# Optimization experiments

Measured on AMD Instinct MI355X. Metric: run time of the kernel, lower is better.

The kernel has to match this reference:

```python
import jax, jax.numpy as jnp
import numpy as np

B, N, D = 8, 256, 256
LN_EPS = 1e-5


def setup_inputs() -> dict:
    key = jax.random.key(0)
    ks = jax.random.split(key, 8)
    s1 = 1.0 / np.sqrt(2 * D)  # torch Linear init scale ~ U(-1/sqrt(fan_in), ...); use normal*scale
    s2 = 1.0 / np.sqrt(D)
    return {
        "patch_features": jax.random.normal(ks[0], (B, N, D), dtype=jnp.float32),
        # relation_transform: Linear(2D, D) -> ReLU -> Linear(D, 1)
        "W1": jax.random.normal(ks[1], (2 * D, D), dtype=jnp.float32) * s1,
        "b1": jax.random.normal(ks[2], (D,), dtype=jnp.float32) * s1,
        "W2": jax.random.normal(ks[3], (D, 1), dtype=jnp.float32) * s2,
        "b2": jax.random.normal(ks[4], (1,), dtype=jnp.float32) * s2,
        # context_projection: Linear(D, D) + LayerNorm(D)
        "Wp": jax.random.normal(ks[5], (D, D), dtype=jnp.float32) * s2,
        "bp": jax.random.normal(ks[6], (D,), dtype=jnp.float32) * s2,
        "ln_gamma": jnp.ones((D,), dtype=jnp.float32),
        "ln_beta": jnp.zeros((D,), dtype=jnp.float32),
    }


def reference(patch_features, W1, b1, W2, b2, Wp, bp, ln_gamma, ln_beta):
    x = patch_features  # [B, N, D]
    d = x.shape[-1]
    # cat([x_i, x_j]) @ W1 == x_i @ W1[:D] + x_j @ W1[D:]
    hi = jnp.einsum("bnd,de->bne", x, W1[:d])   # [B, N, D]
    hj = jnp.einsum("bmd,de->bme", x, W1[d:])   # [B, N, D]
    h = jax.nn.relu(hi[:, :, None, :] + hj[:, None, :, :] + b1)  # [B, N, N, D]
    scores = jnp.einsum("bnmd,do->bnm", h, W2) + b2[0]            # [B, N, N]
    # diagonal entries stay exactly 0 (original never fills i == j)
    eye = jnp.eye(scores.shape[1], dtype=bool)
    scores = jnp.where(eye[None, :, :], 0.0, scores)
    weights = jax.nn.softmax(scores, axis=2)                      # [B, N, N]
    ctx = jnp.einsum("bnm,bmd->bnd", weights, x)                  # [B, N, D]
    proj = jnp.einsum("bnd,de->bne", ctx, Wp) + bp
    mu = jnp.mean(proj, axis=-1, keepdims=True)
    var = jnp.mean(jnp.square(proj - mu), axis=-1, keepdims=True)
    ln = (proj - mu) * jax.lax.rsqrt(var + LN_EPS) * ln_gamma + ln_beta
    return x + ln
```

## Files before the change

### kernel.cpp

```cpp
#include <hip/hip_runtime.h>

#define LN_EPS 1e-5f

__device__ __forceinline__ float wred_max(float v) {
#pragma unroll
    for (int off = 32; off; off >>= 1) v = fmaxf(v, __shfl_xor(v, off, 64));
    return v;
}
__device__ __forceinline__ float wred_sum(float v) {
#pragma unroll
    for (int off = 32; off; off >>= 1) v += __shfl_xor(v, off, 64);
    return v;
}


#define GL(Q, KB) { const float* _p = Wb + (size_t)((KB) * 8) * 256;            \
    _Pragma("unroll") for (int _j = 0; _j < 8; _j++)                            \
        Q[_j] = *(const float2*)(_p + (size_t)_j * 256); }

#define GC(Q, KB) { const int _k = (KB) * 8;                                    \
    _Pragma("unroll") for (int _r = 0; _r < 4; _r++) {                          \
        float4 _xa = *(const float4*)&xs[_r][_k];                               \
        float4 _xb = *(const float4*)&xs[_r][_k + 4];                           \
        acc[_r][0] = fmaf(_xa.x, Q[0].x, acc[_r][0]);                           \
        acc[_r][1] = fmaf(_xa.x, Q[0].y, acc[_r][1]);                           \
        acc[_r][0] = fmaf(_xa.y, Q[1].x, acc[_r][0]);                           \
        acc[_r][1] = fmaf(_xa.y, Q[1].y, acc[_r][1]);                           \
        acc[_r][0] = fmaf(_xa.z, Q[2].x, acc[_r][0]);                           \
        acc[_r][1] = fmaf(_xa.z, Q[2].y, acc[_r][1]);                           \
        acc[_r][0] = fmaf(_xa.w, Q[3].x, acc[_r][0]);                           \
        acc[_r][1] = fmaf(_xa.w, Q[3].y, acc[_r][1]);                           \
        acc[_r][0] = fmaf(_xb.x, Q[4].x, acc[_r][0]);                           \
        acc[_r][1] = fmaf(_xb.x, Q[4].y, acc[_r][1]);                           \
        acc[_r][0] = fmaf(_xb.y, Q[5].x, acc[_r][0]);                           \
        acc[_r][1] = fmaf(_xb.y, Q[5].y, acc[_r][1]);                           \
        acc[_r][0] = fmaf(_xb.z, Q[6].x, acc[_r][0]);                           \
        acc[_r][1] = fmaf(_xb.z, Q[6].y, acc[_r][1]);                           \
        acc[_r][0] = fmaf(_xb.w, Q[7].x, acc[_r][0]);                           \
        acc[_r][1] = fmaf(_xb.w, Q[7].y, acc[_r][1]); } }

__global__ __launch_bounds__(256) void k_gemm_hij(
    const float* __restrict__ x,
    const float* __restrict__ W1,
    const float* __restrict__ b1,
    float* __restrict__ hi_ws,
    float* __restrict__ hjT)
{
    __shared__ __align__(16) float xs[4][256];
    const int t = threadIdx.x;
    const int lane = t & 63, w = t >> 6;
    const int b = blockIdx.x & 7;
    const int i = blockIdx.x >> 3;
    const int row0 = b * 256 + i * 4;

    ((float4*)xs)[t] = ((const float4*)(x + (size_t)row0 * 256))[t];
    __syncthreads();

    const int half = w >> 1;
    const int e0 = ((w & 1) << 7) + 2 * lane;
    const float* Wb = W1 + (size_t)half * 65536 + e0;

    float acc[4][2];
#pragma unroll
    for (int r = 0; r < 4; r++) { acc[r][0] = 0.f; acc[r][1] = 0.f; }

    float2 q[3][8];
    GL(q[0], 0);
    GL(q[1], 1);
#pragma unroll
    for (int kb = 0; kb < 32; kb++) {
        if (kb + 2 < 32) GL(q[(kb + 2) % 3], kb + 2);
        GC(q[kb % 3], kb);
    }

    if (half == 0) {
        float2 bb = *(const float2*)(b1 + e0);
#pragma unroll
        for (int r = 0; r < 4; r++)
            *(float2*)&hi_ws[(size_t)(row0 + r) * 256 + e0] =
                make_float2(acc[r][0] + bb.x, acc[r][1] + bb.y);
    } else {
        const int m0 = i * 4;
        *(float4*)&hjT[(size_t)b * 65536 + (size_t)e0 * 256 + m0] =
            make_float4(acc[0][0], acc[1][0], acc[2][0], acc[3][0]);
        *(float4*)&hjT[(size_t)b * 65536 + (size_t)(e0 + 1) * 256 + m0] =
            make_float4(acc[0][1], acc[1][1], acc[2][1], acc[3][1]);
    }
}


#define P1L(H, G) { const float* _p = hjp + (size_t)((G) * 4) * 256;            \
    _Pragma("unroll") for (int _j = 0; _j < 4; _j++)                            \
        H[_j] = *(const float4*)(_p + (size_t)_j * 256); }

#define P1C(H, G) { const int _db = w * 64 + (G) * 4;                           \
    float4 _wq = *(const float4*)&w2_s[_db];                                    \
    _Pragma("unroll") for (int _n = 0; _n < 4; _n++) {                          \
        float4 _h4 = *(const float4*)&hi_s[_n][_db];                            \
        sp[_n][0] = fmaf(fmaxf(_h4.x + H[0].x, 0.f), _wq.x, sp[_n][0]);         \
        sp[_n][0] = fmaf(fmaxf(_h4.y + H[1].x, 0.f), _wq.y, sp[_n][0]);         \
        sp[_n][0] = fmaf(fmaxf(_h4.z + H[2].x, 0.f), _wq.z, sp[_n][0]);         \
        sp[_n][0] = fmaf(fmaxf(_h4.w + H[3].x, 0.f), _wq.w, sp[_n][0]);         \
        sp[_n][1] = fmaf(fmaxf(_h4.x + H[0].y, 0.f), _wq.x, sp[_n][1]);         \
        sp[_n][1] = fmaf(fmaxf(_h4.y + H[1].y, 0.f), _wq.y, sp[_n][1]);         \
        sp[_n][1] = fmaf(fmaxf(_h4.z + H[2].y, 0.f), _wq.z, sp[_n][1]);         \
        sp[_n][1] = fmaf(fmaxf(_h4.w + H[3].y, 0.f), _wq.w, sp[_n][1]);         \
        sp[_n][2] = fmaf(fmaxf(_h4.x + H[0].z, 0.f), _wq.x, sp[_n][2]);         \
        sp[_n][2] = fmaf(fmaxf(_h4.y + H[1].z, 0.f), _wq.y, sp[_n][2]);         \
        sp[_n][2] = fmaf(fmaxf(_h4.z + H[2].z, 0.f), _wq.z, sp[_n][2]);         \
        sp[_n][2] = fmaf(fmaxf(_h4.w + H[3].z, 0.f), _wq.w, sp[_n][2]);         \
        sp[_n][3] = fmaf(fmaxf(_h4.x + H[0].w, 0.f), _wq.x, sp[_n][3]);         \
        sp[_n][3] = fmaf(fmaxf(_h4.y + H[1].w, 0.f), _wq.y, sp[_n][3]);         \
        sp[_n][3] = fmaf(fmaxf(_h4.z + H[2].w, 0.f), _wq.z, sp[_n][3]);         \
        sp[_n][3] = fmaf(fmaxf(_h4.w + H[3].w, 0.f), _wq.w, sp[_n][3]); } }

#define DL4(X, PTR, G) { const float* _p = (PTR) + (size_t)((G) * 4) * 256;     \
    _Pragma("unroll") for (int _j = 0; _j < 4; _j++)                            \
        X[_j] = *(const float4*)(_p + (size_t)_j * 256); }

#define DC4(ACCV, WS, X, G) { const int _rb = w * 64 + (G) * 4;                 \
    _Pragma("unroll") for (int _n = 0; _n < 4; _n++) {                          \
        float4 _wa = *(const float4*)&WS[_n][_rb];                              \
        ACCV[_n][0] = fmaf(_wa.x, X[0].x, ACCV[_n][0]);                         \
        ACCV[_n][0] = fmaf(_wa.y, X[1].x, ACCV[_n][0]);                         \
        ACCV[_n][0] = fmaf(_wa.z, X[2].x, ACCV[_n][0]);                         \
        ACCV[_n][0] = fmaf(_wa.w, X[3].x, ACCV[_n][0]);                         \
        ACCV[_n][1] = fmaf(_wa.x, X[0].y, ACCV[_n][1]);                         \
        ACCV[_n][1] = fmaf(_wa.y, X[1].y, ACCV[_n][1]);                         \
        ACCV[_n][1] = fmaf(_wa.z, X[2].y, ACCV[_n][1]);                         \
        ACCV[_n][1] = fmaf(_wa.w, X[3].y, ACCV[_n][1]);                         \
        ACCV[_n][2] = fmaf(_wa.x, X[0].z, ACCV[_n][2]);                         \
        ACCV[_n][2] = fmaf(_wa.y, X[1].z, ACCV[_n][2]);                         \
        ACCV[_n][2] = fmaf(_wa.z, X[2].z, ACCV[_n][2]);                         \
        ACCV[_n][2] = fmaf(_wa.w, X[3].z, ACCV[_n][2]);                         \
        ACCV[_n][3] = fmaf(_wa.x, X[0].w, ACCV[_n][3]);                         \
        ACCV[_n][3] = fmaf(_wa.y, X[1].w, ACCV[_n][3]);                         \
        ACCV[_n][3] = fmaf(_wa.z, X[2].w, ACCV[_n][3]);                         \
        ACCV[_n][3] = fmaf(_wa.w, X[3].w, ACCV[_n][3]); } }

__global__ __launch_bounds__(256) void k_fused(
    const float* __restrict__ x,
    const float* __restrict__ hi_ws,
    const float* __restrict__ hjT,
    const float* __restrict__ W2, const float* __restrict__ b2,
    const float* __restrict__ Wp, const float* __restrict__ bp,
    const float* __restrict__ gma, const float* __restrict__ bta,
    float* __restrict__ out)
{
    const int t = threadIdx.x;
    const int lane = t & 63, w = t >> 6;
    const int b = blockIdx.x & 7;
    const int n0 = (blockIdx.x >> 3) * 4;
    const int bn0 = b * 256 + n0;

    __shared__ __align__(16) float hi_s[4][256];
    __shared__ __align__(16) float w2_s[256];
    __shared__ __align__(16) float wt_s[4][256];
    __shared__ __align__(16) float ctx_s[4][256];
    __shared__ __align__(16) float sred[4][4][256];
    __shared__ float part[8][4];

#pragma unroll
    for (int i = 0; i < 4; i++) hi_s[i][t] = hi_ws[(size_t)(bn0 + i) * 256 + t];
    w2_s[t] = W2[t];
    __syncthreads();

    {
        const float* hjp = hjT + (size_t)b * 65536 + (size_t)(w * 64) * 256 + 4 * lane;
        float sp[4][4];
#pragma unroll
        for (int n = 0; n < 4; n++)
#pragma unroll
            for (int j = 0; j < 4; j++) sp[n][j] = 0.f;

        float4 hq[3][4];
        P1L(hq[0], 0);
        P1L(hq[1], 1);
#pragma unroll
        for (int g = 0; g < 16; g++) {
            if (g + 2 < 16) P1L(hq[(g + 2) % 3], g + 2);
            P1C(hq[g % 3], g);
        }

#pragma unroll
        for (int n = 0; n < 4; n++)
            *(float4*)&sred[w][n][4 * lane] =
                make_float4(sp[n][0], sp[n][1], sp[n][2], sp[n][3]);
    }
    __syncthreads();

    float b2v = b2[0];
    float s[4];
#pragma unroll
    for (int i = 0; i < 4; i++) {
        s[i] = ((sred[0][i][t] + sred[1][i][t]) +
                (sred[2][i][t] + sred[3][i][t])) + b2v;
        if (t == n0 + i) s[i] = 0.f;
    }
#pragma unroll
    for (int i = 0; i < 4; i++) {
        float m = wred_max(s[i]);
        if (lane == 0) part[i][w] = m;
    }
    __syncthreads();
    float ev[4];
#pragma unroll
    for (int i = 0; i < 4; i++) {
        float mx = fmaxf(fmaxf(part[i][0], part[i][1]),
                         fmaxf(part[i][2], part[i][3]));
        ev[i] = __expf(s[i] - mx);
        float sm = wred_sum(ev[i]);
        if (lane == 0) part[4 + i][w] = sm;
    }
    __syncthreads();
#pragma unroll
    for (int i = 0; i < 4; i++) {
        float tot = (part[4 + i][0] + part[4 + i][1]) +
                    (part[4 + i][2] + part[4 + i][3]);
        wt_s[i][t] = ev[i] / tot;
    }
    __syncthreads();

    {
        const float* xpp = x + (size_t)b * 65536 + (size_t)(w * 64) * 256 + 4 * lane;
        float cp[4][4];
#pragma unroll
        for (int n = 0; n < 4; n++)
#pragma unroll
            for (int j = 0; j < 4; j++) cp[n][j] = 0.f;

        float4 xq[3][4];
        DL4(xq[0], xpp, 0);
        DL4(xq[1], xpp, 1);
#pragma unroll
        for (int g = 0; g < 16; g++) {
            if (g + 2 < 16) DL4(xq[(g + 2) % 3], xpp, g + 2);
            DC4(cp, wt_s, xq[g % 3], g);
        }

#pragma unroll
        for (int n = 0; n < 4; n++)
            *(float4*)&sred[w][n][4 * lane] =
                make_float4(cp[n][0], cp[n][1], cp[n][2], cp[n][3]);
    }
    __syncthreads();
#pragma unroll
    for (int i = 0; i < 4; i++)
        ctx_s[i][t] = (sred[0][i][t] + sred[1][i][t]) +
                      (sred[2][i][t] + sred[3][i][t]);
    __syncthreads();

    {
        const float* wpp = Wp + (size_t)(w * 64) * 256 + 4 * lane;
        float pq[4][4];
#pragma unroll
        for (int n = 0; n < 4; n++)
#pragma unroll
            for (int j = 0; j < 4; j++) pq[n][j] = 0.f;

        float4 qq[3][4];
        DL4(qq[0], wpp, 0);
        DL4(qq[1], wpp, 1);
#pragma unroll
        for (int g = 0; g < 16; g++) {
            if (g + 2 < 16) DL4(qq[(g + 2) % 3], wpp, g + 2);
            DC4(pq, ctx_s, qq[g % 3], g);
        }

#pragma unroll
        for (int n = 0; n < 4; n++)
            *(float4*)&sred[w][n][4 * lane] =
                make_float4(pq[n][0], pq[n][1], pq[n][2], pq[n][3]);
    }
    __syncthreads();

    float bpv = bp[t];
    float p[4];
#pragma unroll
    for (int i = 0; i < 4; i++)
        p[i] = ((sred[0][i][t] + sred[1][i][t]) +
                (sred[2][i][t] + sred[3][i][t])) + bpv;

#pragma unroll
    for (int i = 0; i < 4; i++) {
        float su = wred_sum(p[i]);
        float sq = wred_sum(p[i] * p[i]);
        if (lane == 0) { part[i][w] = su; part[4 + i][w] = sq; }
    }
    __syncthreads();
    float gv = gma[t], bv = bta[t];
#pragma unroll
    for (int i = 0; i < 4; i++) {
        float su = (part[i][0] + part[i][1]) + (part[i][2] + part[i][3]);
        float sq = (part[4 + i][0] + part[4 + i][1]) +
                   (part[4 + i][2] + part[4 + i][3]);
        float mu = su * (1.f / 256.f);
        float var = sq * (1.f / 256.f) - mu * mu;
        float ln = (p[i] - mu) * rsqrtf(var + LN_EPS) * gv + bv;
        out[(size_t)(bn0 + i) * 256 + t] = x[(size_t)(bn0 + i) * 256 + t] + ln;
    }
}

extern "C" void kernel_launch(void* const* d_in, const int* in_sizes, int n_in,
                              void* d_out, int out_size, void* d_ws, size_t ws_size,
                              hipStream_t stream) {
    const float* x   = (const float*)d_in[0];
    const float* W1  = (const float*)d_in[1];
    const float* b1  = (const float*)d_in[2];
    const float* W2  = (const float*)d_in[3];
    const float* b2  = (const float*)d_in[4];
    const float* Wp  = (const float*)d_in[5];
    const float* bp  = (const float*)d_in[6];
    const float* gma = (const float*)d_in[7];
    const float* bta = (const float*)d_in[8];
    float* out = (float*)d_out;

    float* hi_ws = (float*)d_ws;
    float* hjT   = hi_ws + (size_t)2048 * 256;

    k_gemm_hij<<<512, 256, 0, stream>>>(x, W1, b1, hi_ws, hjT);
    k_fused<<<512, 256, 0, stream>>>(x, hi_ws, hjT, W2, b2, Wp, bp,
                                     gma, bta, out);
}
```

Before: 118.8 us.

## Split fused kernel's reduction dimension across eight waves with 512-thread blocks

```diff
diff --git a/kernel.cpp b/kernel.cpp
--- a/kernel.cpp
+++ b/kernel.cpp
@@ -93,7 +93,7 @@
     _Pragma("unroll") for (int _j = 0; _j < 4; _j++)                            \
         H[_j] = *(const float4*)(_p + (size_t)_j * 256); }
 
-#define P1C(H, G) { const int _db = w * 64 + (G) * 4;                           \
+#define P1C(H, G) { const int _db = w * 32 + (G) * 4;                           \
     float4 _wq = *(const float4*)&w2_s[_db];                                    \
     _Pragma("unroll") for (int _n = 0; _n < 4; _n++) {                          \
         float4 _h4 = *(const float4*)&hi_s[_n][_db];                            \
@@ -118,7 +118,7 @@
     _Pragma("unroll") for (int _j = 0; _j < 4; _j++)                            \
         X[_j] = *(const float4*)(_p + (size_t)_j * 256); }
 
-#define DC4(ACCV, WS, X, G) { const int _rb = w * 64 + (G) * 4;                 \
+#define DC4(ACCV, WS, X, G) { const int _rb = w * 32 + (G) * 4;                 \
     _Pragma("unroll") for (int _n = 0; _n < 4; _n++) {                          \
         float4 _wa = *(const float4*)&WS[_n][_rb];                              \
         ACCV[_n][0] = fmaf(_wa.x, X[0].x, ACCV[_n][0]);                         \
@@ -138,7 +138,7 @@
         ACCV[_n][3] = fmaf(_wa.z, X[2].w, ACCV[_n][3]);                         \
         ACCV[_n][3] = fmaf(_wa.w, X[3].w, ACCV[_n][3]); } }
 
-__global__ __launch_bounds__(256) void k_fused(
+__global__ __launch_bounds__(512, 4) void k_fused(
     const float* __restrict__ x,
     const float* __restrict__ hi_ws,
     const float* __restrict__ hjT,
@@ -157,30 +157,36 @@
     __shared__ __align__(16) float w2_s[256];
     __shared__ __align__(16) float wt_s[4][256];
     __shared__ __align__(16) float ctx_s[4][256];
-    __shared__ __align__(16) float sred[4][4][256];
-    __shared__ float part[8][4];
-
-#pragma unroll
-    for (int i = 0; i < 4; i++) hi_s[i][t] = hi_ws[(size_t)(bn0 + i) * 256 + t];
-    w2_s[t] = W2[t];
+    __shared__ __align__(16) float sred[8][4][256];
+    __shared__ float part[8][8];
+
+    if (t < 256) {
+#pragma unroll
+        for (int i = 0; i < 4; i++)
+            hi_s[i][t] = hi_ws[(size_t)(bn0 + i) * 256 + t];
+        w2_s[t] = W2[t];
+    }
     __syncthreads();
 
     {
-        const float* hjp = hjT + (size_t)b * 65536 + (size_t)(w * 64) * 256 + 4 * lane;
+        const float* hjp = hjT + (size_t)b * 65536 + (size_t)(w * 32) * 256 + 4 * lane;
         float sp[4][4];
 #pragma unroll
         for (int n = 0; n < 4; n++)
 #pragma unroll
             for (int j = 0; j < 4; j++) sp[n][j] = 0.f;
 
-        float4 hq[3][4];
-        P1L(hq[0], 0);
-        P1L(hq[1], 1);
-#pragma unroll
-        for (int g = 0; g < 16; g++) {
-            if (g + 2 < 16) P1L(hq[(g + 2) % 3], g + 2);
-            P1C(hq[g % 3], g);
-        }
+        float4 ha[4], hb[4];
+        P1L(ha, 0);
+        for (int g = 0; g + 2 < 8; g += 2) {
+            P1L(hb, g + 1);
+            P1C(ha, g);
+            P1L(ha, g + 2);
+            P1C(hb, g + 1);
+        }
+        P1L(hb, 7);
+        P1C(ha, 6);
+        P1C(hb, 7);
 
 #pragma unroll
         for (int n = 0; n < 4; n++)
@@ -189,54 +195,64 @@
     }
     __syncthreads();
 
-    float b2v = b2[0];
-    float s[4];
-#pragma unroll
-    for (int i = 0; i < 4; i++) {
-        s[i] = ((sred[0][i][t] + sred[1][i][t]) +
-                (sred[2][i][t] + sred[3][i][t])) + b2v;
-        if (t == n0 + i) s[i] = 0.f;
-    }
-#pragma unroll
-    for (int i = 0; i < 4; i++) {
-        float m = wred_max(s[i]);
-        if (lane == 0) part[i][w] = m;
-    }
-    __syncthreads();
-    float ev[4];
-#pragma unroll
-    for (int i = 0; i < 4; i++) {
-        float mx = fmaxf(fmaxf(part[i][0], part[i][1]),
-                         fmaxf(part[i][2], part[i][3]));
-        ev[i] = __expf(s[i] - mx);
-        float sm = wred_sum(ev[i]);
-        if (lane == 0) part[4 + i][w] = sm;
-    }
-    __syncthreads();
-#pragma unroll
-    for (int i = 0; i < 4; i++) {
-        float tot = (part[4 + i][0] + part[4 + i][1]) +
-                    (part[4 + i][2] + part[4 + i][3]);
-        wt_s[i][t] = ev[i] / tot;
+    float s[4], ev[4];
+    if (t < 256) {
+        float b2v = b2[0];
+#pragma unroll
+        for (int i = 0; i < 4; i++) {
+            s[i] = (((sred[0][i][t] + sred[1][i][t]) +
+                     (sred[2][i][t] + sred[3][i][t])) +
+                    ((sred[4][i][t] + sred[5][i][t]) +
+                     (sred[6][i][t] + sred[7][i][t]))) + b2v;
+            if (t == n0 + i) s[i] = 0.f;
+        }
+#pragma unroll
+        for (int i = 0; i < 4; i++) {
+            float m = wred_max(s[i]);
+            if (lane == 0) part[i][w] = m;
+        }
+    }
+    __syncthreads();
+    if (t < 256) {
+#pragma unroll
+        for (int i = 0; i < 4; i++) {
+            float mx = fmaxf(fmaxf(part[i][0], part[i][1]),
+                             fmaxf(part[i][2], part[i][3]));
+            ev[i] = __expf(s[i] - mx);
+            float sm = wred_sum(ev[i]);
+            if (lane == 0) part[4 + i][w] = sm;
+        }
+    }
+    __syncthreads();
+    if (t < 256) {
+#pragma unroll
+        for (int i = 0; i < 4; i++) {
+            float tot = (part[4 + i][0] + part[4 + i][1]) +
+                        (part[4 + i][2] + part[4 + i][3]);
+            wt_s[i][t] = ev[i] / tot;
+        }
     }
     __syncthreads();
 
     {
-        const float* xpp = x + (size_t)b * 65536 + (size_t)(w * 64) * 256 + 4 * lane;
+        const float* xpp = x + (size_t)b * 65536 + (size_t)(w * 32) * 256 + 4 * lane;
         float cp[4][4];
 #pragma unroll
         for (int n = 0; n < 4; n++)
 #pragma unroll
             for (int j = 0; j < 4; j++) cp[n][j] = 0.f;
 
-        float4 xq[3][4];
-        DL4(xq[0], xpp, 0);
-        DL4(xq[1], xpp, 1);
-#pragma unroll
-        for (int g = 0; g < 16; g++) {
-            if (g + 2 < 16) DL4(xq[(g + 2) % 3], xpp, g + 2);
-            DC4(cp, wt_s, xq[g % 3], g);
-        }
+        float4 xa[4], xb[4];
+        DL4(xa, xpp, 0);
+        for (int g = 0; g + 2 < 8; g += 2) {
+            DL4(xb, xpp, g + 1);
+            DC4(cp, wt_s, xa, g);
+            DL4(xa, xpp, g + 2);
+            DC4(cp, wt_s, xb, g + 1);
+        }
+        DL4(xb, xpp, 7);
+        DC4(cp, wt_s, xa, 6);
+        DC4(cp, wt_s, xb, 7);
 
 #pragma unroll
         for (int n = 0; n < 4; n++)
@@ -244,28 +260,35 @@
                 make_float4(cp[n][0], cp[n][1], cp[n][2], cp[n][3]);
     }
     __syncthreads();
-#pragma unroll
-    for (int i = 0; i < 4; i++)
-        ctx_s[i][t] = (sred[0][i][t] + sred[1][i][t]) +
-                      (sred[2][i][t] + sred[3][i][t]);
+    if (t < 256) {
+#pragma unroll
+        for (int i = 0; i < 4; i++)
+            ctx_s[i][t] = ((sred[0][i][t] + sred[1][i][t]) +
+                           (sred[2][i][t] + sred[3][i][t])) +
+                          ((sred[4][i][t] + sred[5][i][t]) +
+                           (sred[6][i][t] + sred[7][i][t]));
+    }
     __syncthreads();
 
     {
-        const float* wpp = Wp + (size_t)(w * 64) * 256 + 4 * lane;
+        const float* wpp = Wp + (size_t)(w * 32) * 256 + 4 * lane;
         float pq[4][4];
 #pragma unroll
         for (int n = 0; n < 4; n++)
 #pragma unroll
             for (int j = 0; j < 4; j++) pq[n][j] = 0.f;
 
-        float4 qq[3][4];
-        DL4(qq[0], wpp, 0);
-        DL4(qq[1], wpp, 1);
-#pragma unroll
-        for (int g = 0; g < 16; g++) {
-            if (g + 2 < 16) DL4(qq[(g + 2) % 3], wpp, g + 2);
-            DC4(pq, ctx_s, qq[g % 3], g);
-        }
+        float4 qa[4], qb[4];
+        DL4(qa, wpp, 0);
+        for (int g = 0; g + 2 < 8; g += 2) {
+            DL4(qb, wpp, g + 1);
+            DC4(pq, ctx_s, qa, g);
+            DL4(qa, wpp, g + 2);
+            DC4(pq, ctx_s, qb, g + 1);
+        }
+        DL4(qb, wpp, 7);
+        DC4(pq, ctx_s, qa, 6);
+        DC4(pq, ctx_s, qb, 7);
 
 #pragma unroll
         for (int n = 0; n < 4; n++)
@@ -274,30 +297,35 @@
     }
     __syncthreads();
 
-    float bpv = bp[t];
     float p[4];
-#pragma unroll
-    for (int i = 0; i < 4; i++)
-        p[i] = ((sred[0][i][t] + sred[1][i][t]) +
-                (sred[2][i][t] + sred[3][i][t])) + bpv;
-
-#pragma unroll
-    for (int i = 0; i < 4; i++) {
-        float su = wred_sum(p[i]);
-        float sq = wred_sum(p[i] * p[i]);
-        if (lane == 0) { part[i][w] = su; part[4 + i][w] = sq; }
-    }
-    __syncthreads();
-    float gv = gma[t], bv = bta[t];
-#pragma unroll
-    for (int i = 0; i < 4; i++) {
-        float su = (part[i][0] + part[i][1]) + (part[i][2] + part[i][3]);
-        float sq = (part[4 + i][0] + part[4 + i][1]) +
-                   (part[4 + i][2] + part[4 + i][3]);
-        float mu = su * (1.f / 256.f);
-        float var = sq * (1.f / 256.f) - mu * mu;
-        float ln = (p[i] - mu) * rsqrtf(var + LN_EPS) * gv + bv;
-        out[(size_t)(bn0 + i) * 256 + t] = x[(size_t)(bn0 + i) * 256 + t] + ln;
+    if (t < 256) {
+        float bpv = bp[t];
+#pragma unroll
+        for (int i = 0; i < 4; i++)
+            p[i] = (((sred[0][i][t] + sred[1][i][t]) +
+                     (sred[2][i][t] + sred[3][i][t])) +
+                    ((sred[4][i][t] + sred[5][i][t]) +
+                     (sred[6][i][t] + sred[7][i][t]))) + bpv;
+#pragma unroll
+        for (int i = 0; i < 4; i++) {
+            float su = wred_sum(p[i]);
+            float sq = wred_sum(p[i] * p[i]);
+            if (lane == 0) { part[i][w] = su; part[4 + i][w] = sq; }
+        }
+    }
+    __syncthreads();
+    if (t < 256) {
+        float gv = gma[t], bv = bta[t];
+#pragma unroll
+        for (int i = 0; i < 4; i++) {
+            float su = (part[i][0] + part[i][1]) + (part[i][2] + part[i][3]);
+            float sq = (part[4 + i][0] + part[4 + i][1]) +
+                       (part[4 + i][2] + part[4 + i][3]);
+            float mu = su * (1.f / 256.f);
+            float var = sq * (1.f / 256.f) - mu * mu;
+            float ln = (p[i] - mu) * rsqrtf(var + LN_EPS) * gv + bv;
+            out[(size_t)(bn0 + i) * 256 + t] = x[(size_t)(bn0 + i) * 256 + t] + ln;
+        }
     }
 }
 
@@ -319,6 +347,6 @@
     float* hjT   = hi_ws + (size_t)2048 * 256;
 
     k_gemm_hij<<<512, 256, 0, stream>>>(x, W1, b1, hi_ws, hjT);
-    k_fused<<<512, 256, 0, stream>>>(x, hi_ws, hjT, W2, b2, Wp, bp,
+    k_fused<<<512, 512, 0, stream>>>(x, hi_ws, hjT, W2, b2, Wp, bp,
                                      gma, bta, out);
 }
```

Result: slower. 193.8 us (+63.2%).
